# Kernel optimization log

Hardware: AMD Instinct MI355X
Metric: run time of the kernel (lower is better)

## Reference

```python
import jax, jax.numpy as jnp
import numpy as np

B, S, D, H, DH = 4, 1024, 1024, 16, 64  # batch, seq, d_model, heads, head dim (d_Q=d_K=d_V)


def setup_inputs() -> dict:
    key = jax.random.key(0)
    ks = jax.random.split(key, 12)
    std = 0.02
    return {
        "x_Q": jax.random.normal(ks[0], (B, S, D), jnp.float32),
        "x_K": jax.random.normal(ks[1], (B, S, D), jnp.float32),
        "x_V": jax.random.normal(ks[2], (B, S, D), jnp.float32),
        "src_batch_lens": jax.random.randint(ks[3], (B,), 0, S),
        # stacked per-head projection weights: [H, d_model, head_dim]
        "Wq": jax.random.normal(ks[4], (H, D, DH), jnp.float32) * std,
        "bq": jax.random.normal(ks[5], (H, DH), jnp.float32) * std,
        "Wk": jax.random.normal(ks[6], (H, D, DH), jnp.float32) * std,
        "bk": jax.random.normal(ks[7], (H, DH), jnp.float32) * std,
        "Wv": jax.random.normal(ks[8], (H, D, DH), jnp.float32) * std,
        "bv": jax.random.normal(ks[9], (H, DH), jnp.float32) * std,
        "Wo": jax.random.normal(ks[10], (D, D), jnp.float32) * std,
        "bo": jax.random.normal(ks[11], (D,), jnp.float32) * std,
    }


def reference(x_Q, x_K, x_V, src_batch_lens, Wq, bq, Wk, bk, Wv, bv, Wo, bo):
    dq = Wq.shape[-1]
    seq = x_Q.shape[1]
    # all heads at once instead of the per-head python loop
    Q = jnp.einsum('bsd,hde->bhse', x_Q, Wq) + bq[None, :, None, :]
    K = jnp.einsum('bsd,hde->bhse', x_K, Wk) + bk[None, :, None, :]
    V = jnp.einsum('bsd,hde->bhse', x_V, Wv) + bv[None, :, None, :]
    scores = jnp.einsum('bhse,bhte->bhst', Q, K) / jnp.sqrt(jnp.asarray(dq, x_Q.dtype))
    # original: matmul(diag(1..1,0..0), scores) zeroes query rows >= length
    rowmask = (jnp.arange(seq)[None, :] < src_batch_lens[:, None])  # [B, S]
    scores = scores * rowmask[:, None, :, None].astype(scores.dtype)
    A = jax.nn.softmax(scores, axis=-1)  # torch Softmax(dim=2) on [B,S,S] per head = key axis
    AV = jnp.einsum('bhst,bhtv->bhsv', A, V)
    out = AV.transpose(0, 2, 1, 3).reshape(x_Q.shape[0], seq, -1)  # concat heads on dim 2
    return out @ Wo + bo  # dropout p=0 -> identity
```

## Files before the change

### kernel.cpp

```cpp
#include <hip/hip_runtime.h>
#include <stdint.h>

typedef short v8s __attribute__((ext_vector_type(8)));
typedef short v4s __attribute__((ext_vector_type(4)));
typedef float v4f __attribute__((ext_vector_type(4)));

#define AS1 __attribute__((address_space(1)))
#define AS3 __attribute__((address_space(3)))

__device__ __forceinline__ void glds16(const void* g, void* l) {
  __builtin_amdgcn_global_load_lds((const AS1 void*)g, (AS3 void*)l, 16, 0, 0);
}

__device__ __forceinline__ short f2bf(float f) {
  uint32_t u = __float_as_uint(f);
  u += 0x7fffu + ((u >> 16) & 1u);
  return (short)(u >> 16);
}


__global__ __launch_bounds__(256) void cast3_f32_bf16(
    const float* __restrict__ a, const float* __restrict__ b, const float* __restrict__ c,
    short* __restrict__ oa, short* __restrict__ ob, short* __restrict__ oc, int n4) {
  const float* in = (blockIdx.z == 0) ? a : (blockIdx.z == 1) ? b : c;
  short* out      = (blockIdx.z == 0) ? oa : (blockIdx.z == 1) ? ob : oc;
  int i = blockIdx.x * 256 + threadIdx.x;
  if (i < n4) {
    float4 v = ((const float4*)in)[i];
    short4 o = { f2bf(v.x), f2bf(v.y), f2bf(v.z), f2bf(v.w) };
    ((short4*)out)[i] = o;
  }
}

__global__ __launch_bounds__(256) void transpose_w_all(
    const float* __restrict__ wq, const float* __restrict__ wk, const float* __restrict__ wv,
    const float* __restrict__ wo,
    short* __restrict__ oq, short* __restrict__ ok, short* __restrict__ ov,
    short* __restrict__ oo) {
  __shared__ float tile[64][65];
  const int z = blockIdx.z;
  const float* in;
  short* out;
  int C, R, rb, cb;
  if (z < 3) {
    const int slice = blockIdx.y;
    in  = ((z == 0) ? wq : (z == 1) ? wk : wv) + (size_t)slice * 65536;
    out = ((z == 0) ? oq : (z == 1) ? ok : ov) + (size_t)slice * 65536;
    C = 64; R = 1024; rb = blockIdx.x * 64; cb = 0;
  } else {
    in = wo; out = oo;
    C = 1024; R = 1024; rb = blockIdx.x * 64; cb = blockIdx.y * 64;
  }
  int t = threadIdx.x;
  int col = t & 63, r0 = t >> 6;
#pragma unroll
  for (int i = 0; i < 16; ++i) {
    int row = r0 + i * 4;
    tile[row][col] = in[(size_t)(rb + row) * C + cb + col];
  }
  __syncthreads();
#pragma unroll
  for (int i = 0; i < 16; ++i) {
    int orow = r0 + i * 4;
    out[(size_t)(cb + orow) * R + rb + col] = f2bf(tile[col][orow]);
  }
}

template <int MR>
__device__ __forceinline__ void gemm_core(const short* __restrict__ Ag,
                                          const short* __restrict__ Bg,
                                          short* As, short* Bs,
                                          v4f (&acc)[MR / 32][4]) {
  constexpr int MT = MR / 32;
  const int tid  = threadIdx.x;
  const int lane = tid & 63;
  const int w    = tid >> 6;
  const int quad = lane >> 4;
  const int c15  = lane & 15;
  const int wr   = (w >> 1) * (MR / 2);
  const int wc   = (w & 1) * 64;

  const int r0 = tid >> 2, p0 = tid & 3;
  const short* g0 = Ag + (size_t)r0 * 1024 + p0 * 8;
  const short* g1 = g0 + 64 * 1024;
  const short* h0 = Bg + (size_t)r0 * 1024 + p0 * 8;
  const short* h1 = h0 + 64 * 1024;
  short* lA0 = As + tid * 8;
  short* lA1 = As + (256 + tid) * 8;
  short* lB0 = Bs + tid * 8;
  short* lB1 = Bs + (256 + tid) * 8;

  for (int kb = 0; kb < 32; ++kb) {
    __syncthreads();
    glds16(g0, lA0);
    if constexpr (MR == 128) glds16(g1, lA1);
    glds16(h0, lB0); glds16(h1, lB1);
    g0 += 32; h0 += 32; h1 += 32;
    if constexpr (MR == 128) g1 += 32;
    __syncthreads();

    v8s a[MT], b[4];
#pragma unroll
    for (int mt = 0; mt < MT; ++mt)
      a[mt] = *(const v8s*)(As + (wr + mt * 16 + c15) * 32 + quad * 8);
#pragma unroll
    for (int nt = 0; nt < 4; ++nt)
      b[nt] = *(const v8s*)(Bs + (wc + nt * 16 + c15) * 32 + quad * 8);
#pragma unroll
    for (int mt = 0; mt < MT; ++mt)
#pragma unroll
      for (int nt = 0; nt < 4; ++nt)
        acc[mt][nt] = __builtin_amdgcn_mfma_f32_16x16x32_bf16(a[mt], b[nt], acc[mt][nt], 0, 0, 0);
  }
}

__global__ __launch_bounds__(256, 3) void proj_gemm(
    const short* __restrict__ xQ, const short* __restrict__ xK, const short* __restrict__ xV,
    const short* __restrict__ WqT, const short* __restrict__ WkT, const short* __restrict__ WvT,
    const float* __restrict__ bq, const float* __restrict__ bk, const float* __restrict__ bv,
    short* __restrict__ Qb, short* __restrict__ Kb, short* __restrict__ Vtb) {
  __shared__ short As[4096];
  __shared__ short Bs[4096];
  const int lin = blockIdx.x;
  const int z = lin >> 8;
  const int r = lin & 255;
  const int nb = ((r >> 3) & 7) * 128;
  const int mb = (((r & 7) << 2) + (r >> 6)) * 128;
  const short* A    = (z == 0) ? xQ  : (z == 1) ? xK  : xV;
  const short* Bt   = (z == 0) ? WqT : (z == 1) ? WkT : WvT;
  const float* bias = (z == 0) ? bq  : (z == 1) ? bk  : bv;
  short* outp       = (z == 0) ? Qb  : (z == 1) ? Kb  : Vtb;
  v4f acc[4][4] = {};
  gemm_core<128>(A + (size_t)mb * 1024, Bt + (size_t)nb * 1024, As, Bs, acc);

  const int lane = threadIdx.x & 63, w = threadIdx.x >> 6;
  const int quad = lane >> 4, c15 = lane & 15;
  const int wr = (w >> 1) * 64, wc = (w & 1) * 64;
  const bool vmode = (z == 2);
#pragma unroll
  for (int nt = 0; nt < 4; ++nt) {
    const int gn = nb + wc + nt * 16 + c15;
    const float bb = bias[gn];
    const int h = gn >> 6, e = gn & 63;
#pragma unroll
    for (int mt = 0; mt < 4; ++mt) {
      if (!vmode) {
#pragma unroll
        for (int rr = 0; rr < 4; ++rr) {
          const int gm = mb + wr + mt * 16 + quad * 4 + rr;
          const int bi = gm >> 10, s = gm & 1023;
          const size_t base = (size_t)(bi * 16 + h) * 65536;
          outp[base + (size_t)s * 64 + e] = f2bf(acc[mt][nt][rr] + bb);
        }
      } else {
        const int gm0 = mb + wr + mt * 16 + quad * 4;
        const int bi = gm0 >> 10, s0 = gm0 & 1023;
        const size_t base = (size_t)(bi * 16 + h) * 65536;
        short4 st = { f2bf(acc[mt][nt][0] + bb), f2bf(acc[mt][nt][1] + bb),
                      f2bf(acc[mt][nt][2] + bb), f2bf(acc[mt][nt][3] + bb) };
        *(short4*)&outp[base + (size_t)e * 1024 + s0] = st;
      }
    }
  }
}

__global__ __launch_bounds__(256, 3) void out_gemm(
    const short* __restrict__ AV, const short* __restrict__ WoT,
    const float* __restrict__ bo, float* __restrict__ outp) {
  __shared__ short As[2048];
  __shared__ short Bs[4096];
  const int lin = blockIdx.x;
  const int nb = ((lin >> 3) & 7) * 128;
  const int mb = (((lin & 7) << 3) + (lin >> 6)) * 64;
  v4f acc[2][4] = {};
  gemm_core<64>(AV + (size_t)mb * 1024, WoT + (size_t)nb * 1024, As, Bs, acc);
  const int lane = threadIdx.x & 63, w = threadIdx.x >> 6;
  const int quad = lane >> 4, c15 = lane & 15;
  const int wr = (w >> 1) * 32, wc = (w & 1) * 64;
#pragma unroll
  for (int nt = 0; nt < 4; ++nt) {
    const int gn = nb + wc + nt * 16 + c15;
    const float bb = bo[gn];
#pragma unroll
    for (int mt = 0; mt < 2; ++mt)
#pragma unroll
      for (int r = 0; r < 4; ++r) {
        const int gm = mb + wr + mt * 16 + quad * 4 + r;
        outp[(size_t)gm * 1024 + gn] = acc[mt][nt][r] + bb;
      }
  }
}

__global__ __launch_bounds__(256, 2) void attn_kernel(
    const short* __restrict__ Qb, const short* __restrict__ Kb,
    const short* __restrict__ Vtb, const int* __restrict__ lens,
    short* __restrict__ AVb) {
  __shared__ short Ks[2][4096];
  __shared__ short Vs[2][4096];
  const int tid = threadIdx.x, lane = tid & 63, w = tid >> 6;
  const int quad = lane >> 4, c15 = lane & 15;
  const int flat = blockIdx.x;
  const int bh = (flat & 7) + 8 * ((flat >> 3) & 7);
  const int qg = flat >> 6;
  const int b = bh >> 4, h = bh & 15;
  const short* Qp = Qb  + (size_t)bh * 65536;
  const short* Kp = Kb  + (size_t)bh * 65536;
  const short* Vp = Vtb + (size_t)bh * 65536;
  const int len = lens[b];
  const int row0 = qg * 128 + w * 32;

  v8s bq_[2][2];
#pragma unroll
  for (int mg = 0; mg < 2; ++mg)
#pragma unroll
    for (int kf = 0; kf < 2; ++kf)
      bq_[mg][kf] = *(const v8s*)(Qp + (size_t)(row0 + mg * 16 + c15) * 64 + kf * 32 + quad * 8);

  float scale[2];
#pragma unroll
  for (int mg = 0; mg < 2; ++mg)
    scale[mg] = (row0 + mg * 16 + c15 < len) ? 0.125f : 0.0f;

  float sm[2] = { 0.f, 0.f };
  v4f o[2][4] = {};

  const int srow = tid >> 3, spart = tid & 7;
  const int gpart = spart ^ (srow & 7);
  const int kgo0 = srow * 64 + gpart * 8, kgo1 = (srow + 32) * 64 + gpart * 8;
  const int vgo0 = srow * 1024 + gpart * 8, vgo1 = (srow + 32) * 1024 + gpart * 8;
  const int l0 = tid * 8, l1 = 2048 + tid * 8;

  const int c7 = c15 & 7;
  const int krow = c15 * 128;
  const int koff0 = krow + ((quad) ^ c7) * 16;
  const int koff1 = krow + ((4 + quad) ^ c7) * 16;
  const int q2 = quad >> 1, h8 = (quad & 1) * 8;
  int voff[4];
#pragma unroll
  for (int nt = 0; nt < 4; ++nt)
    voff[nt] = krow + ((2 * nt + q2) ^ c7) * 16 + h8;

  glds16(Kp + kgo0, (char*)Ks[0] + l0 * 2);
  glds16(Kp + kgo1, (char*)Ks[0] + l1 * 2);
  glds16(Vp + vgo0, (char*)Vs[0] + l0 * 2);
  glds16(Vp + vgo1, (char*)Vs[0] + l1 * 2);

  for (int kb = 0; kb < 16; ++kb) {
    const int cur = kb & 1, nxt = cur ^ 1;
    __syncthreads();

    if (kb < 15) {
      const short* kt = Kp + (size_t)(kb + 1) * 4096;
      const short* vt = Vp + (kb + 1) * 64;
      glds16(kt + kgo0, (char*)Ks[nxt] + l0 * 2);
      glds16(kt + kgo1, (char*)Ks[nxt] + l1 * 2);
      glds16(vt + vgo0, (char*)Vs[nxt] + l0 * 2);
      glds16(vt + vgo1, (char*)Vs[nxt] + l1 * 2);
    }

    v8s ak[4][2];
#pragma unroll
    for (int nt = 0; nt < 4; ++nt) {
      ak[nt][0] = *(const v8s*)((const char*)Ks[cur] + nt * 2048 + koff0);
      ak[nt][1] = *(const v8s*)((const char*)Ks[cur] + nt * 2048 + koff1);
    }
    v4s av[4][4];
#pragma unroll
    for (int t = 0; t < 4; ++t)
#pragma unroll
      for (int nt = 0; nt < 4; ++nt)
        av[t][nt] = *(const v4s*)((const char*)Vs[cur] + t * 2048 + voff[nt]);

    v4f sc[2][4];
#pragma unroll
    for (int mg = 0; mg < 2; ++mg)
#pragma unroll
      for (int nt = 0; nt < 4; ++nt) {
        v4f z = {};
#pragma unroll
        for (int kf = 0; kf < 2; ++kf)
          z = __builtin_amdgcn_mfma_f32_16x16x32_bf16(ak[nt][kf], bq_[mg][kf], z, 0, 0, 0);
        sc[mg][nt] = z;
      }

    v4s pb[2][4];
#pragma unroll
    for (int mg = 0; mg < 2; ++mg)
#pragma unroll
      for (int nt = 0; nt < 4; ++nt) {
        v4s pv;
#pragma unroll
        for (int r = 0; r < 4; ++r) {
          float p = __expf(sc[mg][nt][r] * scale[mg]);
          sm[mg] += p;
          pv[r] = f2bf(p);
        }
        pb[mg][nt] = pv;
      }

#pragma unroll
    for (int mg = 0; mg < 2; ++mg)
#pragma unroll
      for (int t = 0; t < 4; ++t)
#pragma unroll
        for (int nt = 0; nt < 4; ++nt)
          o[mg][t] = __builtin_amdgcn_mfma_f32_16x16x16bf16_1k(av[t][nt], pb[mg][nt], o[mg][t], 0, 0, 0);
  }

#pragma unroll
  for (int mg = 0; mg < 2; ++mg) {
    sm[mg] += __shfl_xor(sm[mg], 16);
    sm[mg] += __shfl_xor(sm[mg], 32);
  }

#pragma unroll
  for (int mg = 0; mg < 2; ++mg) {
    const float inv = 1.0f / sm[mg];
    const size_t rowbase = (size_t)(b * 1024 + row0 + mg * 16 + c15) * 1024 + h * 64;
#pragma unroll
    for (int t = 0; t < 4; ++t) {
      short4 st = { f2bf(o[mg][t][0] * inv), f2bf(o[mg][t][1] * inv),
                    f2bf(o[mg][t][2] * inv), f2bf(o[mg][t][3] * inv) };
      *(short4*)&AVb[rowbase + t * 16 + quad * 4] = st;
    }
  }
}

extern "C" void kernel_launch(void* const* d_in, const int* in_sizes, int n_in,
                              void* d_out, int out_size, void* d_ws, size_t ws_size,
                              hipStream_t stream) {
  const float* xQ = (const float*)d_in[0];
  const float* xK = (const float*)d_in[1];
  const float* xV = (const float*)d_in[2];
  const int* lens = (const int*)d_in[3];
  const float* Wq = (const float*)d_in[4];
  const float* bq = (const float*)d_in[5];
  const float* Wk = (const float*)d_in[6];
  const float* bk = (const float*)d_in[7];
  const float* Wv = (const float*)d_in[8];
  const float* bv = (const float*)d_in[9];
  const float* Wo = (const float*)d_in[10];
  const float* bo = (const float*)d_in[11];
  float* out = (float*)d_out;

  char* ws = (char*)d_ws;
  short* xQb = (short*)(ws + 0);
  short* xKb = (short*)(ws + 8388608);
  short* xVb = (short*)(ws + 16777216);
  short* WqT = (short*)(ws + 25165824);
  short* WkT = (short*)(ws + 27262976);
  short* WvT = (short*)(ws + 29360128);
  short* WoT = (short*)(ws + 31457280);
  short* Qb  = (short*)(ws + 33554432);
  short* Kb  = (short*)(ws + 41943040);
  short* Vtb = (short*)(ws + 50331648);
  short* AVb = (short*)(ws + 58720256);

  cast3_f32_bf16<<<dim3(4096, 1, 3), 256, 0, stream>>>(xQ, xK, xV, xQb, xKb, xVb, 1048576);
  transpose_w_all<<<dim3(16, 16, 4), 256, 0, stream>>>(Wq, Wk, Wv, Wo, WqT, WkT, WvT, WoT);
  proj_gemm<<<dim3(768), 256, 0, stream>>>(xQb, xKb, xVb, WqT, WkT, WvT,
                                           bq, bk, bv, Qb, Kb, Vtb);
  attn_kernel<<<dim3(512), 256, 0, stream>>>(Qb, Kb, Vtb, lens, AVb);
  out_gemm<<<dim3(512), 256, 0, stream>>>(AVb, WoT, bo, out);
}
```

Before: 205.3 us.

## Triple-buffer GEMM LDS tiles with two-ahead async prefetch

The shared GEMM core now keeps three LDS buffers and issues global-to-LDS loads two k-tiles ahead. It uses an explicit vmcnt wait plus a single barrier per iteration instead of two syncthreads. This is meant to hide global load latency behind MFMA work in the projection and output GEMMs. LDS use per block triples, which may limit occupancy, and the tail iterations issue redundant loads.

```diff
diff --git a/kernel.cpp b/kernel.cpp
--- a/kernel.cpp
+++ b/kernel.cpp
@@ -72,6 +72,8 @@
                                           short* As, short* Bs,
                                           v4f (&acc)[MR / 32][4]) {
   constexpr int MT = MR / 32;
+  constexpr int ASZ = MR * 32;
+  constexpr int BSZ = 128 * 32;
   const int tid  = threadIdx.x;
   const int lane = tid & 63;
   const int w    = tid >> 6;
@@ -81,31 +83,43 @@
   const int wc   = (w & 1) * 64;
 
   const int r0 = tid >> 2, p0 = tid & 3;
-  const short* g0 = Ag + (size_t)r0 * 1024 + p0 * 8;
-  const short* g1 = g0 + 64 * 1024;
-  const short* h0 = Bg + (size_t)r0 * 1024 + p0 * 8;
-  const short* h1 = h0 + 64 * 1024;
-  short* lA0 = As + tid * 8;
-  short* lA1 = As + (256 + tid) * 8;
-  short* lB0 = Bs + tid * 8;
-  short* lB1 = Bs + (256 + tid) * 8;
+  const short* a0 = Ag + (size_t)r0 * 1024 + p0 * 8;
+  const short* a1 = a0 + 64 * 1024;
+  const short* b0 = Bg + (size_t)r0 * 1024 + p0 * 8;
+  const short* b1 = b0 + 64 * 1024;
+  short* lA = As + tid * 8;
+  short* lB = Bs + tid * 8;
+
+  auto issue = [&](int t, int buf) {
+    const int o = t * 32;
+    glds16(a0 + o, lA + buf * ASZ);
+    if constexpr (MR == 128) glds16(a1 + o, lA + buf * ASZ + 2048);
+    glds16(b0 + o, lB + buf * BSZ);
+    glds16(b1 + o, lB + buf * BSZ + 2048);
+  };
+
+  issue(0, 0);
+  issue(1, 1);
 
   for (int kb = 0; kb < 32; ++kb) {
-    __syncthreads();
-    glds16(g0, lA0);
-    if constexpr (MR == 128) glds16(g1, lA1);
-    glds16(h0, lB0); glds16(h1, lB1);
-    g0 += 32; h0 += 32; h1 += 32;
-    if constexpr (MR == 128) g1 += 32;
-    __syncthreads();
+    if constexpr (MR == 128)
+      asm volatile("s_waitcnt vmcnt(4)\n\ts_barrier" ::: "memory");
+    else
+      asm volatile("s_waitcnt vmcnt(3)\n\ts_barrier" ::: "memory");
+
+    const int t2 = kb + 2;
+    issue(t2 < 32 ? t2 : 31, t2 % 3);
+
+    const short* Ab = As + (kb % 3) * ASZ;
+    const short* Bb = Bs + (kb % 3) * BSZ;
 
     v8s a[MT], b[4];
 #pragma unroll
     for (int mt = 0; mt < MT; ++mt)
-      a[mt] = *(const v8s*)(As + (wr + mt * 16 + c15) * 32 + quad * 8);
+      a[mt] = *(const v8s*)(Ab + (wr + mt * 16 + c15) * 32 + quad * 8);
 #pragma unroll
     for (int nt = 0; nt < 4; ++nt)
-      b[nt] = *(const v8s*)(Bs + (wc + nt * 16 + c15) * 32 + quad * 8);
+      b[nt] = *(const v8s*)(Bb + (wc + nt * 16 + c15) * 32 + quad * 8);
 #pragma unroll
     for (int mt = 0; mt < MT; ++mt)
 #pragma unroll
@@ -119,8 +133,8 @@
     const short* __restrict__ WqT, const short* __restrict__ WkT, const short* __restrict__ WvT,
     const float* __restrict__ bq, const float* __restrict__ bk, const float* __restrict__ bv,
     short* __restrict__ Qb, short* __restrict__ Kb, short* __restrict__ Vtb) {
-  __shared__ short As[4096];
-  __shared__ short Bs[4096];
+  __shared__ short As[12288];
+  __shared__ short Bs[12288];
   const int lin = blockIdx.x;
   const int z = lin >> 8;
   const int r = lin & 255;
@@ -167,8 +181,8 @@
 __global__ __launch_bounds__(256, 3) void out_gemm(
     const short* __restrict__ AV, const short* __restrict__ WoT,
     const float* __restrict__ bo, float* __restrict__ outp) {
-  __shared__ short As[2048];
-  __shared__ short Bs[4096];
+  __shared__ short As[6144];
+  __shared__ short Bs[12288];
   const int lin = blockIdx.x;
   const int nb = ((lin >> 3) & 7) * 128;
   const int mb = (((lin & 7) << 3) + (lin >> 6)) * 64;
```

Measured after the change: 204.9 us. Within noise of the previous version (-0.2%).
